# Performance work log

Hardware: AMD Instinct MI355X
Metric: run time of the kernel (lower is better)

The kernel has to match this reference:

```python
import jax, jax.numpy as jnp
import numpy as np

N_NODES = 50000
N_EDGES = 800000
HID = 64
N_GRAPHS = 64


def setup_inputs() -> dict:
    key = jax.random.key(0)
    ks = jax.random.split(key, 12)
    x = jax.random.normal(ks[0], (N_NODES, 1), dtype=jnp.float32)
    edge_index = jax.random.randint(ks[1], (2, N_EDGES), 0, N_NODES, dtype=jnp.int64)
    batch = jnp.sort(jax.random.randint(ks[2], (N_NODES,), 0, N_GRAPHS, dtype=jnp.int64))
    def glorot(k, shape):
        fan_in, fan_out = shape
        s = jnp.sqrt(2.0 / (fan_in + fan_out)).astype(jnp.float32)
        return jax.random.normal(k, shape, dtype=jnp.float32) * s
    return {
        "x": x, "edge_index": edge_index, "batch": batch,
        "W1l": glorot(ks[3], (1, HID)), "b1": jnp.zeros((HID,), jnp.float32), "W1r": glorot(ks[4], (1, HID)),
        "W2l": glorot(ks[5], (HID, HID)), "b2": jnp.zeros((HID,), jnp.float32), "W2r": glorot(ks[6], (HID, HID)),
        "W3l": glorot(ks[7], (HID, HID)), "b3": jnp.zeros((HID,), jnp.float32), "W3r": glorot(ks[8], (HID, HID)),
        "Wfc1": glorot(ks[9], (HID, HID // 2)), "bfc1": jnp.zeros((HID // 2,), jnp.float32),
        "Wfc2": glorot(ks[10], (HID // 2, 1)), "bfc2": jnp.zeros((1,), jnp.float32),
    }


def _sage_conv(x, src, dst, Wl, bl, Wr):
    # PyG SAGEConv (mean aggr): lin_l(mean_{j in N(i)} x_j) + lin_r(x_i)
    msgs = x[src]                                                   # [E, d] gather
    agg = jax.ops.segment_sum(msgs, dst, num_segments=N_NODES)      # [N, d] scatter-add
    cnt = jax.ops.segment_sum(jnp.ones((src.shape[0], 1), x.dtype), dst, num_segments=N_NODES)
    mean = agg / jnp.maximum(cnt, 1.0)                              # isolated nodes -> 0
    return mean @ Wl + bl + x @ Wr


def reference(x, edge_index, batch,
              W1l, b1, W1r, W2l, b2, W2r, W3l, b3, W3r,
              Wfc1, bfc1, Wfc2, bfc2):
    src, dst = edge_index[0], edge_index[1]
    layers = [(W1l, b1, W1r), (W2l, b2, W2r), (W3l, b3, W3r)]
    h = x
    for (Wl, bl, Wr) in layers:
        h_res = h
        h = jax.nn.relu(_sage_conv(h, src, dst, Wl, bl, Wr))
        # dropout is identity at inference; residual broadcasts [N,64]+[N,1] on layer 1
        h = h + h_res
    # global mean pool over graphs in the batch
    sums = jax.ops.segment_sum(h, batch, num_segments=N_GRAPHS)     # [G, d]
    cnts = jax.ops.segment_sum(jnp.ones((h.shape[0], 1), h.dtype), batch, num_segments=N_GRAPHS)
    pooled = sums / jnp.maximum(cnts, 1.0)
    out = jax.nn.relu(pooled @ Wfc1 + bfc1)
    out = out @ Wfc2 + bfc2                                          # [G, 1]
    return out
```

## Files before the change

### kernel.cpp

```cpp
#include <hip/hip_runtime.h>
#include <hip/hip_bf16.h>
#include <hip/hip_fp16.h>

#define HID 64
#define NGRAPHS 64
#define BUCKET 64
#define CAP 4096
#define EPB 2048
#define NSLOT 33

typedef _Float16 half8 __attribute__((ext_vector_type(8)));
typedef float floatx4 __attribute__((ext_vector_type(4)));
typedef float floatx2 __attribute__((ext_vector_type(2)));

__device__ __forceinline__ unsigned char enc_fp8(float v) {
    int pk = __builtin_amdgcn_cvt_pk_fp8_f32(v, v, 0, false);
    return (unsigned char)(pk & 0xff);
}

__device__ __forceinline__ void cvt_acc16(float* bank, const uint4& u) {
    floatx2 p;
    p = __builtin_amdgcn_cvt_pk_f32_fp8(u.x, false); bank[0] += p[0];  bank[1] += p[1];
    p = __builtin_amdgcn_cvt_pk_f32_fp8(u.x, true);  bank[2] += p[0];  bank[3] += p[1];
    p = __builtin_amdgcn_cvt_pk_f32_fp8(u.y, false); bank[4] += p[0];  bank[5] += p[1];
    p = __builtin_amdgcn_cvt_pk_f32_fp8(u.y, true);  bank[6] += p[0];  bank[7] += p[1];
    p = __builtin_amdgcn_cvt_pk_f32_fp8(u.z, false); bank[8] += p[0];  bank[9] += p[1];
    p = __builtin_amdgcn_cvt_pk_f32_fp8(u.z, true);  bank[10] += p[0]; bank[11] += p[1];
    p = __builtin_amdgcn_cvt_pk_f32_fp8(u.w, false); bank[12] += p[0]; bank[13] += p[1];
    p = __builtin_amdgcn_cvt_pk_f32_fp8(u.w, true);  bank[14] += p[0]; bank[15] += p[1];
}

__global__ __launch_bounds__(256) void detect_init_kernel(const void* edge, const void* batch,
                                                          int* flags, int* bcursor,
                                                          float* psum,
                                                          const float* W2l, const float* W2r,
                                                          const float* W3l, const float* W3r,
                                                          __half* wl2f, __half* wr2f,
                                                          __half* wl3f, __half* wr3f,
                                                          int E2, int N, int G, int NB) {
    int t = threadIdx.x;
    int b = blockIdx.x;
    if (b == 0) {
        for (int i = t; i < NB; i += 256) bcursor[i] = i * CAP;
        for (int i = t; i < G * HID; i += 256) psum[i] = 0.0f;
        if (t < 64) {
            int lane = t;
            int half_ = E2 / 2;
            int stride = half_ / 64; if (stride < 1) stride = 1;
            int j = lane * stride; if (j >= half_) j = half_ - 1;
            long long v = ((const long long*)edge)[j];
            bool ok = (v >= 0 && v < (long long)N);
            unsigned long long m = __ballot(ok);
            if (lane == 0) flags[0] = (m == ~0ULL) ? 1 : 0;
            int halfB = N / 2;
            int strideB = halfB / 64; if (strideB < 1) strideB = 1;
            int jb = lane * strideB; if (jb >= halfB) jb = halfB - 1;
            long long vb = ((const long long*)batch)[jb];
            bool okb = (vb >= 0 && vb < (long long)G);
            unsigned long long mb = __ballot(okb);
            if (lane == 0) flags[1] = (mb == ~0ULL) ? 1 : 0;
        }
    } else {
        const float* src = (b == 1) ? W2l : (b == 2) ? W2r : (b == 3) ? W3l : W3r;
        __half* dst = (b == 1) ? wl2f : (b == 2) ? wr2f : (b == 3) ? wl3f : wr3f;
        for (int i = t; i < HID * HID; i += 256) {
            int j = i & 7;
            int lane = (i >> 3) & 63;
            int nt = (i >> 9) & 3;
            int kh = i >> 11;
            int k = kh * 32 + (lane >> 4) * 8 + j;
            int col = nt * 16 + (lane & 15);
            dst[i] = __float2half(src[k * HID + col]);
        }
    }
}

__device__ __forceinline__ int idx_at(const void* p, int i, bool is64) {
    return is64 ? (int)((const long long*)p)[i] : ((const int*)p)[i];
}

__global__ __launch_bounds__(256) void bin_scatter_kernel(const void* edge, const int* __restrict__ flags,
                                                          int* __restrict__ bcursor,
                                                          unsigned int* __restrict__ entries,
                                                          int E, int NB) {
    extern __shared__ int lds[];
    int* hist = lds;
    int* base = lds + NB;
    int* ssrc = lds + 2 * NB;
    int* sdst = ssrc + EPB;
    for (int i = threadIdx.x; i < NB; i += 256) hist[i] = 0;
    __syncthreads();
    bool is64 = flags[0] != 0;
    int start = blockIdx.x * EPB;
    int end = start + EPB; if (end > E) end = E;
    int cnt = end - start;
    for (int k = threadIdx.x; k < cnt; k += 256) {
        int e = start + k;
        int srcv = idx_at(edge, e, is64);
        int d = idx_at(edge, E + e, is64);
        ssrc[k] = srcv;
        sdst[k] = d;
        atomicAdd(&hist[d >> 6], 1);
    }
    __syncthreads();
    for (int i = threadIdx.x; i < NB; i += 256) {
        int h = hist[i];
        base[i] = h ? atomicAdd(&bcursor[i], h) : 0;
    }
    __syncthreads();
    for (int i = threadIdx.x; i < NB; i += 256) hist[i] = 0;
    __syncthreads();
    for (int k = threadIdx.x; k < cnt; k += 256) {
        int d = sdst[k];
        int b = d >> 6;
        int lo = atomicAdd(&hist[b], 1);
        int p = base[b] + lo;
        if (p < (b + 1) * CAP)
            entries[p] = ((unsigned int)ssrc[k] << 6) | (unsigned int)(d & 63);
    }
}

__global__ __launch_bounds__(256) void csr_l1_kernel(const unsigned int* __restrict__ entries,
                                                     const int* __restrict__ bcursor,
                                                     const float* __restrict__ x,
                                                     const float* __restrict__ W1l,
                                                     const float* __restrict__ b1,
                                                     const float* __restrict__ W1r,
                                                     int* __restrict__ rowptr,
                                                     int* __restrict__ deg,
                                                     int* __restrict__ csr,
                                                     __half* __restrict__ h1h,
                                                     unsigned char* __restrict__ h1q,
                                                     int N, int NB) {
    __shared__ int hist[BUCKET];
    __shared__ int lstart[BUCKET];
    __shared__ int lcur[BUCKET];
    __shared__ float accx[BUCKET];
    __shared__ float sx[BUCKET];
    int t = threadIdx.x;
    int b = blockIdx.x;
    int r0 = b * CAP;
    int cnt = bcursor[b] - r0; if (cnt > CAP) cnt = CAP;
    if (t < BUCKET) {
        hist[t] = 0; lcur[t] = 0; accx[t] = 0.0f;
        int node = b * BUCKET + t;
        sx[t] = (node < N) ? x[node] : 0.0f;
    }
    __syncthreads();
    for (int j = r0 + t; j < r0 + cnt; j += 256) {
        unsigned int en = entries[j];
        atomicAdd(&hist[en & 63u], 1);
        atomicAdd(&accx[en & 63u], x[en >> 6]);
    }
    __syncthreads();
    if (t < BUCKET) {
        int v = hist[t];
        int s = v;
#pragma unroll
        for (int off = 1; off < 64; off <<= 1) {
            int u = __shfl_up(s, off);
            if (t >= off) s += u;
        }
        lstart[t] = s - v;
        int node = b * BUCKET + t;
        if (node < N) {
            rowptr[node] = r0 + s - v;
            deg[node] = v;
        }
    }
    __syncthreads();
    for (int j = r0 + t; j < r0 + cnt; j += 256) {
        unsigned int en = entries[j];
        int dl = (int)(en & 63u);
        int p = atomicAdd(&lcur[dl], 1);
        csr[r0 + lstart[dl] + p] = (int)(en >> 6);
    }
    __syncthreads();
    int f = t & 63;
    int sub = t >> 6;
    float wlf = W1l[f], bf = b1[f], wrf = W1r[f];
    for (int it = 0; it < 16; ++it) {
        int nl = it * 4 + sub;
        int node = b * BUCKET + nl;
        if (node < N) {
            int d = hist[nl];
            float mv = (d > 0) ? accx[nl] / (float)d : 0.0f;
            float xv = sx[nl];
            float v = fmaf(mv, wlf, fmaf(xv, wrf, bf));
            v = v > 0.0f ? v : 0.0f;
            float hv = v + xv;
            h1h[(size_t)node * HID + f] = __float2half(hv);
            h1q[(size_t)node * HID + f] = enc_fp8(hv);
        }
    }
}

__global__ __launch_bounds__(256) void gather_mfma_kernel(const int* __restrict__ rowptr,
                                                          const int* __restrict__ deg,
                                                          const int* __restrict__ csr,
                                                          const unsigned char* __restrict__ hq,
                                                          const __half* __restrict__ hph,
                                                          const __half* __restrict__ Wlf,
                                                          const float* __restrict__ bvec,
                                                          const __half* __restrict__ Wrf,
                                                          __half* __restrict__ houth,
                                                          unsigned char* __restrict__ houtq,
                                                          float* __restrict__ psum,
                                                          const void* batch,
                                                          const int* __restrict__ flags,
                                                          int N) {
    extern __shared__ char dynlds[];
    _Float16 (*smean)[HID + 8] = (_Float16 (*)[HID + 8])dynlds;
    float (*spool)[HID] = (float (*)[HID])(dynlds + 64 * (HID + 8) * 2);
    int* sb = (int*)(dynlds + 64 * (HID + 8) * 2 + NSLOT * HID * 4);
    int t = threadIdx.x;
    bool pool = (psum != nullptr);
    if (pool) {
        for (int i = t; i < NSLOT * HID; i += 256) ((float*)spool)[i] = 0.0f;
        if (t < 64) {
            int node = blockIdx.x * 64 + t;
            sb[t] = (node < N) ? idx_at(batch, node, flags[1] != 0) : -1;
        }
    }

    {
        int grp = t >> 2;
        int l = t & 3;
        int i = blockIdx.x * 64 + grp;
        if (i < N) {
            int r0 = rowptr[i];
            int d = deg[i];
            int r1 = r0 + d;
            float a0[16], a1[16];
#pragma unroll
            for (int k = 0; k < 16; ++k) { a0[k] = 0.0f; a1[k] = 0.0f; }
            int j = r0;
            for (; j + 16 <= r1; j += 16) {
                uint4 u[16];
#pragma unroll
                for (int m = 0; m < 16; ++m) {
                    int s = csr[j + m];
                    u[m] = *(const uint4*)(hq + (size_t)s * HID + l * 16);
                }
#pragma unroll
                for (int m = 0; m < 16; ++m) cvt_acc16((m & 1) ? a1 : a0, u[m]);
            }
            if (j < r1) {
                uint4 u[16];
#pragma unroll
                for (int m = 0; m < 16; ++m) {
                    int jm = j + m;
                    bool ok = jm < r1;
                    int s = csr[ok ? jm : r0];
                    uint4 v = *(const uint4*)(hq + (size_t)s * HID + l * 16);
                    u[m].x = ok ? v.x : 0u;
                    u[m].y = ok ? v.y : 0u;
                    u[m].z = ok ? v.z : 0u;
                    u[m].w = ok ? v.w : 0u;
                }
#pragma unroll
                for (int m = 0; m < 16; ++m) cvt_acc16((m & 1) ? a1 : a0, u[m]);
            }
            float inv = (d > 0) ? 1.0f / (float)d : 0.0f;
            __half2 o[8];
#pragma unroll
            for (int q = 0; q < 8; ++q)
                o[q] = __floats2half2_rn((a0[2 * q] + a1[2 * q]) * inv,
                                         (a0[2 * q + 1] + a1[2 * q + 1]) * inv);
            uint4* dst = (uint4*)&smean[grp][l * 16];
            dst[0] = ((uint4*)o)[0];
            dst[1] = ((uint4*)o)[1];
        }
    }
    __syncthreads();

    int wave = t >> 6;
    int lane = t & 63;
    int m = lane & 15;
    int quad = lane >> 4;
    int node0 = blockIdx.x * 64 + wave * 16;
    if (node0 < N) {
        const _Float16* wlp = (const _Float16*)Wlf;
        const _Float16* wrp = (const _Float16*)Wrf;
        half8 bl[2][4], br[2][4];
#pragma unroll
        for (int kh = 0; kh < 2; ++kh)
#pragma unroll
            for (int nt = 0; nt < 4; ++nt) {
                size_t off = (size_t)((kh * 4 + nt) * 64 + lane) * 8;
                bl[kh][nt] = *(const half8*)(wlp + off);
                br[kh][nt] = *(const half8*)(wrp + off);
            }
        int nlA = wave * 16 + m;
        half8 am0 = *(const half8*)&smean[nlA][quad * 8];
        half8 am1 = *(const half8*)&smean[nlA][32 + quad * 8];
        int nodeA = node0 + m; if (nodeA >= N) nodeA = N - 1;
        const _Float16* hrow = (const _Float16*)hph + (size_t)nodeA * HID;
        half8 ah0 = *(const half8*)(hrow + quad * 8);
        half8 ah1 = *(const half8*)(hrow + 32 + quad * 8);

#pragma unroll
        for (int nt = 0; nt < 4; ++nt) {
            float b = bvec[nt * 16 + m];
            floatx4 c = {b, b, b, b};
            c = __builtin_amdgcn_mfma_f32_16x16x32_f16(am0, bl[0][nt], c, 0, 0, 0);
            c = __builtin_amdgcn_mfma_f32_16x16x32_f16(am1, bl[1][nt], c, 0, 0, 0);
            c = __builtin_amdgcn_mfma_f32_16x16x32_f16(ah0, br[0][nt], c, 0, 0, 0);
            c = __builtin_amdgcn_mfma_f32_16x16x32_f16(ah1, br[1][nt], c, 0, 0, 0);
            int f = nt * 16 + m;
#pragma unroll
            for (int r = 0; r < 4; ++r) {
                int nodeR = node0 + quad * 4 + r;
                if (nodeR < N) {
                    float v = c[r];
                    v = v > 0.0f ? v : 0.0f;
                    v += __half2float(((const __half*)hph)[(size_t)nodeR * HID + f]);
                    if (!pool) {
                        houth[(size_t)nodeR * HID + f] = __float2half(v);
                        houtq[(size_t)nodeR * HID + f] = enc_fp8(v);
                    } else {
                        int bg = sb[wave * 16 + quad * 4 + r];
                        int slot = bg - sb[0];
                        if (slot < NSLOT) atomicAdd(&spool[slot][f], v);
                        else atomicAdd(&psum[bg * HID + f], v);
                    }
                }
            }
        }
    }

    if (pool) {
        __syncthreads();
        int gbase = sb[0];
        for (int i = t; i < NSLOT * HID; i += 256) {
            int s = i >> 6, f = i & 63;
            float v = spool[s][f];
            if (v != 0.0f) atomicAdd(&psum[(gbase + s) * HID + f], v);
        }
    }
}

__device__ __forceinline__ int lbound(const void* batch, int n, long long key, bool is64) {
    int lo = 0, hi = n;
    while (lo < hi) {
        int mid = (lo + hi) >> 1;
        long long v = is64 ? ((const long long*)batch)[mid] : (long long)((const int*)batch)[mid];
        if (v < key) lo = mid + 1; else hi = mid;
    }
    return lo;
}

__global__ __launch_bounds__(64) void fc_kernel(const float* __restrict__ psum,
                                                const void* batch,
                                                const int* __restrict__ flags,
                                                const float* __restrict__ Wfc1,
                                                const float* __restrict__ bfc1,
                                                const float* __restrict__ Wfc2,
                                                const float* __restrict__ bfc2,
                                                float* __restrict__ out, int N) {
    __shared__ int sb2[2];
    __shared__ float mean[HID];
    int g = blockIdx.x;
    int t = threadIdx.x;
    bool is64 = flags[1] != 0;
    if (t == 0) sb2[0] = lbound(batch, N, g, is64);
    if (t == 1) sb2[1] = lbound(batch, N, g + 1, is64);
    __syncthreads();
    float c = fmaxf((float)(sb2[1] - sb2[0]), 1.0f);
    mean[t] = psum[g * HID + t] / c;
    __syncthreads();
    float v = 0.0f;
    if (t < 32) {
        float acc = bfc1[t];
#pragma unroll
        for (int k = 0; k < HID; ++k) acc += mean[k] * Wfc1[k * 32 + t];
        float hcc = acc > 0.0f ? acc : 0.0f;
        v = hcc * Wfc2[t];
    }
#pragma unroll
    for (int off = 32; off >= 1; off >>= 1) v += __shfl_down(v, off);
    if (t == 0) out[g] = v + bfc2[0];
}

extern "C" void kernel_launch(void* const* d_in, const int* in_sizes, int n_in,
                              void* d_out, int out_size, void* d_ws, size_t ws_size,
                              hipStream_t stream) {
    const int N = in_sizes[0];
    const int E2 = in_sizes[1];
    const int E = E2 / 2;
    const int NB = (N + BUCKET - 1) / BUCKET;

    const float* x    = (const float*)d_in[0];
    const void*  edge = d_in[1];
    const void*  batch= d_in[2];
    const float* W1l  = (const float*)d_in[3];
    const float* b1   = (const float*)d_in[4];
    const float* W1r  = (const float*)d_in[5];
    const float* W2l  = (const float*)d_in[6];
    const float* b2   = (const float*)d_in[7];
    const float* W2r  = (const float*)d_in[8];
    const float* W3l  = (const float*)d_in[9];
    const float* b3   = (const float*)d_in[10];
    const float* W3r  = (const float*)d_in[11];
    const float* Wfc1 = (const float*)d_in[12];
    const float* bfc1 = (const float*)d_in[13];
    const float* Wfc2 = (const float*)d_in[14];
    const float* bfc2 = (const float*)d_in[15];
    float* out = (float*)d_out;

    char* ws = (char*)d_ws;
    size_t o = 0;
    auto alloc = [&](size_t bytes) { char* p = ws + o; o += (bytes + 255) & ~(size_t)255; return p; };
    int*   bcursor = (int*)alloc((size_t)NB * 4);
    float* psum    = (float*)alloc((size_t)NGRAPHS * HID * 4);
    unsigned int* entries = (unsigned int*)alloc((size_t)NB * CAP * 4);
    int*   csr     = (int*)alloc((size_t)NB * CAP * 4);
    int*   rowptr  = (int*)alloc((size_t)N * 4);
    int*   deg     = (int*)alloc((size_t)N * 4);
    __half* h1h    = (__half*)alloc((size_t)N * HID * 2);
    __half* h2h    = (__half*)alloc((size_t)N * HID * 2);
    unsigned char* h1q = (unsigned char*)alloc((size_t)N * HID);
    unsigned char* h2q = (unsigned char*)alloc((size_t)N * HID);
    __half* wl2f   = (__half*)alloc((size_t)HID * HID * 2);
    __half* wr2f   = (__half*)alloc((size_t)HID * HID * 2);
    __half* wl3f   = (__half*)alloc((size_t)HID * HID * 2);
    __half* wr3f   = (__half*)alloc((size_t)HID * HID * 2);
    int*   flags   = (int*)alloc(16);

    detect_init_kernel<<<5, 256, 0, stream>>>(edge, batch, flags, bcursor, psum,
                                              W2l, W2r, W3l, W3r, wl2f, wr2f, wl3f, wr3f,
                                              E2, N, NGRAPHS, NB);

    const int nblk = (E + EPB - 1) / EPB;
    const int scatter_lds = (2 * NB + 2 * EPB) * 4;
    bin_scatter_kernel<<<nblk, 256, scatter_lds, stream>>>(edge, flags, bcursor, entries, E, NB);

    csr_l1_kernel<<<NB, 256, 0, stream>>>(entries, bcursor, x, W1l, b1, W1r,
                                          rowptr, deg, csr, h1h, h1q, N, NB);

    const int fusedBlocks = (N + 63) / 64;
    const int smeanBytes = 64 * (HID + 8) * 2;
    const int poolBytes  = smeanBytes + NSLOT * HID * 4 + 64 * 4;

    gather_mfma_kernel<<<fusedBlocks, 256, smeanBytes, stream>>>(rowptr, deg, csr, h1q, h1h,
                                                                 wl2f, b2, wr2f, h2h, h2q,
                                                                 (float*)nullptr, nullptr, flags, N);

    gather_mfma_kernel<<<fusedBlocks, 256, poolBytes, stream>>>(rowptr, deg, csr, h2q, h2h,
                                                                wl3f, b3, wr3f, (__half*)nullptr,
                                                                (unsigned char*)nullptr,
                                                                psum, batch, flags, N);

    fc_kernel<<<NGRAPHS, 64, 0, stream>>>(psum, batch, flags, Wfc1, bfc1, Wfc2, bfc2, out, N);
}
```

Baseline: 192.9 us.

## Split fused gather+MFMA layer into separate gather and MFMA kernels

The fused per-layer kernel is split in two. A small 64-thread gather kernel writes the mean-aggregated fp16 features to a global buffer, and a separate 256-thread MFMA kernel reads that buffer for the linear transforms, residual and pooling. The aim is to let the latency-bound gather run at higher occupancy with finer blocks, without the LDS staging and block-wide barrier. In exchange it adds an extra global write and read of an N×64 fp16 buffer plus two more kernel launches.

```diff
diff --git a/kernel.cpp b/kernel.cpp
--- a/kernel.cpp
+++ b/kernel.cpp
@@ -195,24 +195,74 @@
     }
 }
 
-__global__ __launch_bounds__(256) void gather_mfma_kernel(const int* __restrict__ rowptr,
-                                                          const int* __restrict__ deg,
-                                                          const int* __restrict__ csr,
-                                                          const unsigned char* __restrict__ hq,
-                                                          const __half* __restrict__ hph,
-                                                          const __half* __restrict__ Wlf,
-                                                          const float* __restrict__ bvec,
-                                                          const __half* __restrict__ Wrf,
-                                                          __half* __restrict__ houth,
-                                                          unsigned char* __restrict__ houtq,
-                                                          float* __restrict__ psum,
-                                                          const void* batch,
-                                                          const int* __restrict__ flags,
-                                                          int N) {
-    extern __shared__ char dynlds[];
-    _Float16 (*smean)[HID + 8] = (_Float16 (*)[HID + 8])dynlds;
-    float (*spool)[HID] = (float (*)[HID])(dynlds + 64 * (HID + 8) * 2);
-    int* sb = (int*)(dynlds + 64 * (HID + 8) * 2 + NSLOT * HID * 4);
+__global__ __launch_bounds__(64, 2) void gather_kernel(const int* __restrict__ rowptr,
+                                                       const int* __restrict__ deg,
+                                                       const int* __restrict__ csr,
+                                                       const unsigned char* __restrict__ hq,
+                                                       __half* __restrict__ gmean,
+                                                       int N) {
+    int t = threadIdx.x;
+    int grp = t >> 2;
+    int l = t & 3;
+    int node = blockIdx.x * 16 + grp;
+    if (node >= N) return;
+    int r0 = rowptr[node];
+    int d = deg[node];
+    int r1 = r0 + d;
+    float a0[16], a1[16];
+#pragma unroll
+    for (int k = 0; k < 16; ++k) { a0[k] = 0.0f; a1[k] = 0.0f; }
+    int j = r0;
+    for (; j + 16 <= r1; j += 16) {
+        uint4 u[16];
+#pragma unroll
+        for (int m = 0; m < 16; ++m) {
+            int s = csr[j + m];
+            u[m] = *(const uint4*)(hq + (size_t)s * HID + l * 16);
+        }
+#pragma unroll
+        for (int m = 0; m < 16; ++m) cvt_acc16((m & 1) ? a1 : a0, u[m]);
+    }
+    if (j < r1) {
+        uint4 u[16];
+#pragma unroll
+        for (int m = 0; m < 16; ++m) {
+            int jm = j + m;
+            bool ok = jm < r1;
+            int s = csr[ok ? jm : r0];
+            uint4 v = *(const uint4*)(hq + (size_t)s * HID + l * 16);
+            u[m].x = ok ? v.x : 0u;
+            u[m].y = ok ? v.y : 0u;
+            u[m].z = ok ? v.z : 0u;
+            u[m].w = ok ? v.w : 0u;
+        }
+#pragma unroll
+        for (int m = 0; m < 16; ++m) cvt_acc16((m & 1) ? a1 : a0, u[m]);
+    }
+    float inv = (d > 0) ? 1.0f / (float)d : 0.0f;
+    __half2 o[8];
+#pragma unroll
+    for (int q = 0; q < 8; ++q)
+        o[q] = __floats2half2_rn((a0[2 * q] + a1[2 * q]) * inv,
+                                 (a0[2 * q + 1] + a1[2 * q + 1]) * inv);
+    uint4* dst = (uint4*)((_Float16*)gmean + (size_t)node * HID + l * 16);
+    dst[0] = ((uint4*)o)[0];
+    dst[1] = ((uint4*)o)[1];
+}
+
+__global__ __launch_bounds__(256) void mfma_kernel(const __half* __restrict__ gmean,
+                                                   const __half* __restrict__ hph,
+                                                   const __half* __restrict__ Wlf,
+                                                   const float* __restrict__ bvec,
+                                                   const __half* __restrict__ Wrf,
+                                                   __half* __restrict__ houth,
+                                                   unsigned char* __restrict__ houtq,
+                                                   float* __restrict__ psum,
+                                                   const void* batch,
+                                                   const int* __restrict__ flags,
+                                                   int N) {
+    __shared__ float spool[NSLOT][HID];
+    __shared__ int sb[64];
     int t = threadIdx.x;
     bool pool = (psum != nullptr);
     if (pool) {
@@ -221,58 +271,8 @@
             int node = blockIdx.x * 64 + t;
             sb[t] = (node < N) ? idx_at(batch, node, flags[1] != 0) : -1;
         }
-    }
-
-    {
-        int grp = t >> 2;
-        int l = t & 3;
-        int i = blockIdx.x * 64 + grp;
-        if (i < N) {
-            int r0 = rowptr[i];
-            int d = deg[i];
-            int r1 = r0 + d;
-            float a0[16], a1[16];
-#pragma unroll
-            for (int k = 0; k < 16; ++k) { a0[k] = 0.0f; a1[k] = 0.0f; }
-            int j = r0;
-            for (; j + 16 <= r1; j += 16) {
-                uint4 u[16];
-#pragma unroll
-                for (int m = 0; m < 16; ++m) {
-                    int s = csr[j + m];
-                    u[m] = *(const uint4*)(hq + (size_t)s * HID + l * 16);
-                }
-#pragma unroll
-                for (int m = 0; m < 16; ++m) cvt_acc16((m & 1) ? a1 : a0, u[m]);
-            }
-            if (j < r1) {
-                uint4 u[16];
-#pragma unroll
-                for (int m = 0; m < 16; ++m) {
-                    int jm = j + m;
-                    bool ok = jm < r1;
-                    int s = csr[ok ? jm : r0];
-                    uint4 v = *(const uint4*)(hq + (size_t)s * HID + l * 16);
-                    u[m].x = ok ? v.x : 0u;
-                    u[m].y = ok ? v.y : 0u;
-                    u[m].z = ok ? v.z : 0u;
-                    u[m].w = ok ? v.w : 0u;
-                }
-#pragma unroll
-                for (int m = 0; m < 16; ++m) cvt_acc16((m & 1) ? a1 : a0, u[m]);
-            }
-            float inv = (d > 0) ? 1.0f / (float)d : 0.0f;
-            __half2 o[8];
-#pragma unroll
-            for (int q = 0; q < 8; ++q)
-                o[q] = __floats2half2_rn((a0[2 * q] + a1[2 * q]) * inv,
-                                         (a0[2 * q + 1] + a1[2 * q + 1]) * inv);
-            uint4* dst = (uint4*)&smean[grp][l * 16];
-            dst[0] = ((uint4*)o)[0];
-            dst[1] = ((uint4*)o)[1];
-        }
-    }
-    __syncthreads();
+        __syncthreads();
+    }
 
     int wave = t >> 6;
     int lane = t & 63;
@@ -291,10 +291,10 @@
                 bl[kh][nt] = *(const half8*)(wlp + off);
                 br[kh][nt] = *(const half8*)(wrp + off);
             }
-        int nlA = wave * 16 + m;
-        half8 am0 = *(const half8*)&smean[nlA][quad * 8];
-        half8 am1 = *(const half8*)&smean[nlA][32 + quad * 8];
         int nodeA = node0 + m; if (nodeA >= N) nodeA = N - 1;
+        const _Float16* grow = (const _Float16*)gmean + (size_t)nodeA * HID;
+        half8 am0 = *(const half8*)(grow + quad * 8);
+        half8 am1 = *(const half8*)(grow + 32 + quad * 8);
         const _Float16* hrow = (const _Float16*)hph + (size_t)nodeA * HID;
         half8 ah0 = *(const half8*)(hrow + quad * 8);
         half8 ah1 = *(const half8*)(hrow + 32 + quad * 8);
@@ -419,6 +419,7 @@
     int*   deg     = (int*)alloc((size_t)N * 4);
     __half* h1h    = (__half*)alloc((size_t)N * HID * 2);
     __half* h2h    = (__half*)alloc((size_t)N * HID * 2);
+    __half* gmean  = (__half*)alloc((size_t)N * HID * 2);
     unsigned char* h1q = (unsigned char*)alloc((size_t)N * HID);
     unsigned char* h2q = (unsigned char*)alloc((size_t)N * HID);
     __half* wl2f   = (__half*)alloc((size_t)HID * HID * 2);
@@ -438,18 +439,17 @@
     csr_l1_kernel<<<NB, 256, 0, stream>>>(entries, bcursor, x, W1l, b1, W1r,
                                           rowptr, deg, csr, h1h, h1q, N, NB);
 
-    const int fusedBlocks = (N + 63) / 64;
-    const int smeanBytes = 64 * (HID + 8) * 2;
-    const int poolBytes  = smeanBytes + NSLOT * HID * 4 + 64 * 4;
-
-    gather_mfma_kernel<<<fusedBlocks, 256, smeanBytes, stream>>>(rowptr, deg, csr, h1q, h1h,
-                                                                 wl2f, b2, wr2f, h2h, h2q,
-                                                                 (float*)nullptr, nullptr, flags, N);
-
-    gather_mfma_kernel<<<fusedBlocks, 256, poolBytes, stream>>>(rowptr, deg, csr, h2q, h2h,
-                                                                wl3f, b3, wr3f, (__half*)nullptr,
-                                                                (unsigned char*)nullptr,
-                                                                psum, batch, flags, N);
+    const int gatherBlocks = (N + 15) / 16;
+    const int mfmaBlocks   = (N + 63) / 64;
+
+    gather_kernel<<<gatherBlocks, 64, 0, stream>>>(rowptr, deg, csr, h1q, gmean, N);
+    mfma_kernel<<<mfmaBlocks, 256, 0, stream>>>(gmean, h1h, wl2f, b2, wr2f, h2h, h2q,
+                                                (float*)nullptr, nullptr, flags, N);
+
+    gather_kernel<<<gatherBlocks, 64, 0, stream>>>(rowptr, deg, csr, h2q, gmean, N);
+    mfma_kernel<<<mfmaBlocks, 256, 0, stream>>>(gmean, h2h, wl3f, b3, wr3f, (__half*)nullptr,
+                                                (unsigned char*)nullptr,
+                                                psum, batch, flags, N);
 
     fc_kernel<<<NGRAPHS, 64, 0, stream>>>(psum, batch, flags, Wfc1, bfc1, Wfc2, bfc2, out, N);
 }
```

New measurement: 193.6 us. About the same (+0.3%).
